# Optimization experiments

Hardware: AMD Instinct MI355X
Metric: run time of the kernel (lower is better)

## Reference

```python
import jax, jax.numpy as jnp
import numpy as np

BETA = 1.0
POWER_ITERS = 9
EPS = 1e-12  # F.normalize default eps


def _normalize(v):
    # L2 normalize over dim=1 of [B, N, 1], matching F.normalize(x, dim=1)
    n = jnp.linalg.norm(v, axis=1, keepdims=True)
    return v / jnp.maximum(n, EPS)


def _dominant_eigenvalue(A, x):
    # A: [B, N, N], x: [B, N, 1]
    for _ in range(POWER_ITERS):
        x = _normalize(jnp.matmul(A, x))
    Ax = jnp.matmul(A, x)[..., 0]              # [B, N]
    num = jnp.sum(Ax * x[..., 0], axis=1)      # x^T A x
    den = jnp.sum(x[..., 0] ** 2, axis=1)      # ||x||^2 (== 1 after normalize)
    return num / den, x


def setup_inputs() -> dict:
    key = jax.random.key(0)
    k1, k2 = jax.random.split(key)
    B, C, H, W = 256, 2048, 7, 7
    x = jax.random.normal(k1, (B, C, H, W), dtype=jnp.float32)
    x0 = _normalize(jax.random.normal(k2, (B, H * W, 1), dtype=jnp.float32))
    return {"x": x, "x0": x0}


def reference(x, x0):
    B, C, H, W = x.shape
    N = H * W
    Wm = x.reshape(B, C, N)
    # ATA = W^T W : [B, N, N]
    ATA = jnp.einsum('bcn,bcm->bnm', Wm, Wm)
    # first power iteration: largest eigenvalue; x0 is a no_grad constant
    largest, x1 = _dominant_eigenvalue(ATA, jax.lax.stop_gradient(x0))
    I = jnp.eye(N, dtype=ATA.dtype)
    shifted = ATA - largest[:, None, None] * I
    # second power iteration warm-started from detached x1 (torch stores last_x detached)
    tmp, _ = _dominant_eigenvalue(shifted, jax.lax.stop_gradient(x1))
    smallest = tmp + largest
    penalty = BETA * (largest / smallest - 1.0) ** 2
    return jnp.sum(penalty) / B
```

## Files before the change

### kernel.cpp

```cpp
#include <hip/hip_runtime.h>
#include <hip/hip_bf16.h>
#include <stdint.h>


#define BATCH 256
#define CDIM  2048
#define NDIM  49
#define QK    512
#define NQ    4
#define CHUNK 64
#define NCHUNK (QK / CHUNK)
#define ITEMS (NDIM * (CHUNK / 8))
#define PSTRIDE 2404

typedef __bf16 bf16x8 __attribute__((ext_vector_type(8)));
typedef float  f32x16 __attribute__((ext_vector_type(16)));
typedef float  f32x4  __attribute__((ext_vector_type(4)));

union V16 {
  f32x4  f4;
  bf16x8 b8;
};

__device__ __forceinline__ void load8(const float* __restrict__ g,
                                      float (&r)[8]) {
#pragma unroll
  for (int j = 0; j < 8; ++j) r[j] = g[j * NDIM];
}

__device__ __forceinline__ void cvt_store(const float (&r)[8], uint32_t* Hb,
                                          uint32_t* Lb, int w) {
  bf16x8 hv, lv;
#pragma unroll
  for (int j = 0; j < 8; ++j) {
    float e = r[j];
    __bf16 h = (__bf16)e;
    hv[j] = h;
    lv[j] = (__bf16)(e - (float)h);
  }
  V16 a, b;
  a.b8 = hv;
  b.b8 = lv;
  *(f32x4*)(Hb + w) = a.f4;
  *(f32x4*)(Lb + w) = b.f4;
}

__device__ __forceinline__ void comp16(const uint32_t* Hb, const uint32_t* Lb,
                                       int m, int n, int hf, f32x16& c1,
                                       f32x16& c2, f32x16& c3) {
  const f32x4* H = (const f32x4*)Hb;
  const f32x4* L = (const f32x4*)Lb;
#pragma unroll
  for (int s = 0; s < 4; ++s) {
    const int blk = 2 * s + hf;
    V16 ah, al, bh, bl;
    ah.f4 = H[m * 8 + (blk ^ (m & 7))];
    al.f4 = L[m * 8 + (blk ^ (m & 7))];
    bh.f4 = H[n * 8 + (blk ^ (n & 7))];
    bl.f4 = L[n * 8 + (blk ^ (n & 7))];
    c1 = __builtin_amdgcn_mfma_f32_32x32x16_bf16(ah.b8, bh.b8, c1, 0, 0, 0);
    c2 = __builtin_amdgcn_mfma_f32_32x32x16_bf16(ah.b8, bl.b8, c2, 0, 0, 0);
    c3 = __builtin_amdgcn_mfma_f32_32x32x16_bf16(al.b8, bh.b8, c3, 0, 0, 0);
  }
}

__global__ __launch_bounds__(256, 4) void gram_kernel(
    const float* __restrict__ x, float* __restrict__ partial,
    float* __restrict__ out) {
  __shared__ __align__(16) uint32_t ldsHi[2][2048];
  __shared__ __align__(16) uint32_t ldsLo[2][2048];

  const int tid  = threadIdx.x;
  const int bidx = blockIdx.x;
  const int batch = bidx >> 2;
  const int q     = bidx & 3;
  const int lane = tid & 63;
  const int wv   = tid >> 6;
  const int ln   = lane & 31;
  const int hf   = lane >> 5;
  const int qm = wv >> 1, qn = wv & 1;
  const int m = qm * 32 + ln;
  const int n = qn * 32 + ln;

  if (bidx == 0 && tid == 0) out[0] = 0.f;

  const float* gbase = x + (size_t)batch * (CDIM * NDIM)
                         + (size_t)q * (QK * NDIM);

  const int i0 = tid;
  const int i1 = tid + 256;
  const bool v1 = (i1 < ITEMS);
  const int kq0 = (i0 * 1338) >> 16;
  const int n0  = i0 - 49 * kq0;
  const int kq1 = (i1 * 1338) >> 16;
  const int n1  = i1 - 49 * kq1;
  const int g0  = kq0 * (8 * NDIM) + n0;
  const int g1  = kq1 * (8 * NDIM) + n1;
  const int w0  = n0 * 32 + 4 * (kq0 ^ (n0 & 7));
  const int w1  = n1 * 32 + 4 * (kq1 ^ (n1 & 7));

  f32x16 c1, c2, c3;
#pragma unroll
  for (int i = 0; i < 16; ++i) { c1[i] = 0.f; c2[i] = 0.f; c3[i] = 0.f; }

  float sA0[8], sA1[8], sB0[8], sB1[8];

  load8(gbase + g0, sA0);
  if (v1) load8(gbase + g1, sA1);

#pragma unroll
  for (int ch = 0; ch < NCHUNK; ch += 2) {
    {
      const float* gch = gbase + (size_t)(ch + 1) * (CHUNK * NDIM);
      load8(gch + g0, sB0);
      if (v1) load8(gch + g1, sB1);
    }
    cvt_store(sA0, ldsHi[0], ldsLo[0], w0);
    if (v1) cvt_store(sA1, ldsHi[0], ldsLo[0], w1);
    __syncthreads();
    comp16(ldsHi[0], ldsLo[0], m, n, hf, c1, c2, c3);

    if (ch + 2 < NCHUNK) {
      const float* gch = gbase + (size_t)(ch + 2) * (CHUNK * NDIM);
      load8(gch + g0, sA0);
      if (v1) load8(gch + g1, sA1);
    }
    cvt_store(sB0, ldsHi[1], ldsLo[1], w0);
    if (v1) cvt_store(sB1, ldsHi[1], ldsLo[1], w1);
    __syncthreads();
    comp16(ldsHi[1], ldsLo[1], m, n, hf, c1, c2, c3);
  }

  float* outp = partial + (size_t)bidx * PSTRIDE;
#pragma unroll
  for (int r = 0; r < 16; ++r) {
    int row = (r & 3) + 8 * (r >> 2) + 4 * hf;
    int mm = qm * 32 + row;
    if (mm < NDIM && n < NDIM)
      outp[mm * NDIM + n] = c1[r] + c2[r] + c3[r];
  }
}

__global__ __launch_bounds__(256) void eigen_kernel(
    const float* __restrict__ partial, const float* __restrict__ x0,
    float* __restrict__ out) {
  __shared__ __align__(16) float A[NDIM * NDIM + 3];

  const int b = blockIdx.x;
  const int t = threadIdx.x;
  const float* p0 = partial + (size_t)(NQ * b) * PSTRIDE;

  const f32x4* q0 = (const f32x4*)(p0);
  const f32x4* q1 = (const f32x4*)(p0 + PSTRIDE);
  const f32x4* q2 = (const f32x4*)(p0 + 2 * PSTRIDE);
  const f32x4* q3 = (const f32x4*)(p0 + 3 * PSTRIDE);
  for (int i = t; i < 600; i += 256) {
    f32x4 s = q0[i] + q1[i] + q2[i] + q3[i];
    ((f32x4*)A)[i] = s;
  }
  if (t == 0)
    A[2400] = p0[2400] + p0[PSTRIDE + 2400] + p0[2 * PSTRIDE + 2400] +
              p0[3 * PSTRIDE + 2400];
  __syncthreads();

  if (t < 64) {
    const bool act = (t < NDIM);
    float Ar[NDIM];
    {
      const float* Arow = &A[(act ? t : (NDIM - 1)) * NDIM];
#pragma unroll
      for (int k = 0; k < NDIM; ++k) Ar[k] = Arow[k];
    }
    float xl = act ? x0[b * NDIM + t] : 0.f;

    auto rayleigh = [&](float shift) -> float {
      for (int it = 0; it < 9; ++it) {
        float a0 = 0.f, a1 = 0.f, a2 = 0.f, a3 = 0.f;
#pragma unroll
        for (int k = 0; k < 48; k += 4) {
          a0 = fmaf(Ar[k + 0], __shfl(xl, k + 0, 64), a0);
          a1 = fmaf(Ar[k + 1], __shfl(xl, k + 1, 64), a1);
          a2 = fmaf(Ar[k + 2], __shfl(xl, k + 2, 64), a2);
          a3 = fmaf(Ar[k + 3], __shfl(xl, k + 3, 64), a3);
        }
        a0 = fmaf(Ar[48], __shfl(xl, 48, 64), a0);
        float y = act ? (((a0 + a1) + (a2 + a3)) - shift * xl) : 0.f;
        float s2 = y * y;
#pragma unroll
        for (int o = 32; o; o >>= 1) s2 += __shfl_xor(s2, o, 64);
        xl = y / fmaxf(sqrtf(s2), 1e-12f);
      }
      float a0 = 0.f, a1 = 0.f, a2 = 0.f, a3 = 0.f;
#pragma unroll
      for (int k = 0; k < 48; k += 4) {
        a0 = fmaf(Ar[k + 0], __shfl(xl, k + 0, 64), a0);
        a1 = fmaf(Ar[k + 1], __shfl(xl, k + 1, 64), a1);
        a2 = fmaf(Ar[k + 2], __shfl(xl, k + 2, 64), a2);
        a3 = fmaf(Ar[k + 3], __shfl(xl, k + 3, 64), a3);
      }
      a0 = fmaf(Ar[48], __shfl(xl, 48, 64), a0);
      float yy = act ? (((a0 + a1) + (a2 + a3)) - shift * xl) : 0.f;
      float num = yy * xl;
      float den = xl * xl;
#pragma unroll
      for (int o = 32; o; o >>= 1) {
        num += __shfl_xor(num, o, 64);
        den += __shfl_xor(den, o, 64);
      }
      return num / den;
    };

    float largest  = rayleigh(0.f);
    float smallest = rayleigh(largest) + largest;
    if (t == 0) {
      float r = largest / smallest - 1.f;
      atomicAdd(out, r * r * (1.0f / (float)BATCH));
    }
  }
}

extern "C" void kernel_launch(void* const* d_in, const int* in_sizes, int n_in,
                              void* d_out, int out_size, void* d_ws,
                              size_t ws_size, hipStream_t stream) {
  const float* x  = (const float*)d_in[0];
  const float* x0 = (const float*)d_in[1];
  float* out = (float*)d_out;
  float* partial = (float*)d_ws;

  gram_kernel<<<1024, 256, 0, stream>>>(x, partial, out);
  eigen_kernel<<<BATCH, 256, 0, stream>>>(partial, x0, out);
}
```

Before: 172.0 us.

## Fuse Gram computation and eigen iteration into one block per batch

Removes the 4-way channel split of the Gram matrix. Each of 256 blocks now computes the full 49x49 Gram matrix for one batch over all 2048 channels, writes it to shared memory, and runs both power iterations in the same kernel. The global partial-sum buffer, the separate eigen kernel and the atomicAdd are gone, replaced by a per-batch penalty array and a small one-block reduction kernel. This saves the partial round trip and a launch, but cuts the grid from 1024 to 256 blocks, which lowers parallelism for the memory-bound Gram phase. Each block also runs a serial loop four times longer.

New measurement: 172.8 us. No clear change (+0.5%).

```diff
diff --git a/kernel.cpp b/kernel.cpp
--- a/kernel.cpp
+++ b/kernel.cpp
@@ -6,12 +6,10 @@
 #define BATCH 256
 #define CDIM  2048
 #define NDIM  49
-#define QK    512
-#define NQ    4
 #define CHUNK 64
-#define NCHUNK (QK / CHUNK)
+#define NCHUNK (CDIM / CHUNK)
 #define ITEMS (NDIM * (CHUNK / 8))
-#define PSTRIDE 2404
+#define CHUNK_FLOATS (CHUNK * NDIM)
 
 typedef __bf16 bf16x8 __attribute__((ext_vector_type(8)));
 typedef float  f32x16 __attribute__((ext_vector_type(16)));
@@ -64,16 +62,15 @@
   }
 }
 
-__global__ __launch_bounds__(256, 4) void gram_kernel(
-    const float* __restrict__ x, float* __restrict__ partial,
-    float* __restrict__ out) {
+__global__ __launch_bounds__(256) void fused_kernel(
+    const float* __restrict__ x, const float* __restrict__ x0,
+    float* __restrict__ pen) {
   __shared__ __align__(16) uint32_t ldsHi[2][2048];
   __shared__ __align__(16) uint32_t ldsLo[2][2048];
+  __shared__ __align__(16) float A[NDIM * NDIM + 3];
 
   const int tid  = threadIdx.x;
-  const int bidx = blockIdx.x;
-  const int batch = bidx >> 2;
-  const int q     = bidx & 3;
+  const int b    = blockIdx.x;
   const int lane = tid & 63;
   const int wv   = tid >> 6;
   const int ln   = lane & 31;
@@ -82,10 +79,7 @@
   const int m = qm * 32 + ln;
   const int n = qn * 32 + ln;
 
-  if (bidx == 0 && tid == 0) out[0] = 0.f;
-
-  const float* gbase = x + (size_t)batch * (CDIM * NDIM)
-                         + (size_t)q * (QK * NDIM);
+  const float* gbase = x + (size_t)b * (CDIM * NDIM);
 
   const int i0 = tid;
   const int i1 = tid + 256;
@@ -108,10 +102,9 @@
   load8(gbase + g0, sA0);
   if (v1) load8(gbase + g1, sA1);
 
-#pragma unroll
   for (int ch = 0; ch < NCHUNK; ch += 2) {
     {
-      const float* gch = gbase + (size_t)(ch + 1) * (CHUNK * NDIM);
+      const float* gch = gbase + (size_t)(ch + 1) * CHUNK_FLOATS;
       load8(gch + g0, sB0);
       if (v1) load8(gch + g1, sB1);
     }
@@ -121,7 +114,7 @@
     comp16(ldsHi[0], ldsLo[0], m, n, hf, c1, c2, c3);
 
     if (ch + 2 < NCHUNK) {
-      const float* gch = gbase + (size_t)(ch + 2) * (CHUNK * NDIM);
+      const float* gch = gbase + (size_t)(ch + 2) * CHUNK_FLOATS;
       load8(gch + g0, sA0);
       if (v1) load8(gch + g1, sA1);
     }
@@ -131,47 +124,24 @@
     comp16(ldsHi[1], ldsLo[1], m, n, hf, c1, c2, c3);
   }
 
-  float* outp = partial + (size_t)bidx * PSTRIDE;
 #pragma unroll
   for (int r = 0; r < 16; ++r) {
     int row = (r & 3) + 8 * (r >> 2) + 4 * hf;
     int mm = qm * 32 + row;
     if (mm < NDIM && n < NDIM)
-      outp[mm * NDIM + n] = c1[r] + c2[r] + c3[r];
-  }
-}
-
-__global__ __launch_bounds__(256) void eigen_kernel(
-    const float* __restrict__ partial, const float* __restrict__ x0,
-    float* __restrict__ out) {
-  __shared__ __align__(16) float A[NDIM * NDIM + 3];
-
-  const int b = blockIdx.x;
-  const int t = threadIdx.x;
-  const float* p0 = partial + (size_t)(NQ * b) * PSTRIDE;
-
-  const f32x4* q0 = (const f32x4*)(p0);
-  const f32x4* q1 = (const f32x4*)(p0 + PSTRIDE);
-  const f32x4* q2 = (const f32x4*)(p0 + 2 * PSTRIDE);
-  const f32x4* q3 = (const f32x4*)(p0 + 3 * PSTRIDE);
-  for (int i = t; i < 600; i += 256) {
-    f32x4 s = q0[i] + q1[i] + q2[i] + q3[i];
-    ((f32x4*)A)[i] = s;
-  }
-  if (t == 0)
-    A[2400] = p0[2400] + p0[PSTRIDE + 2400] + p0[2 * PSTRIDE + 2400] +
-              p0[3 * PSTRIDE + 2400];
+      A[mm * NDIM + n] = c1[r] + c2[r] + c3[r];
+  }
   __syncthreads();
 
-  if (t < 64) {
-    const bool act = (t < NDIM);
+  if (tid < 64) {
+    const bool act = (tid < NDIM);
     float Ar[NDIM];
     {
-      const float* Arow = &A[(act ? t : (NDIM - 1)) * NDIM];
+      const float* Arow = &A[(act ? tid : (NDIM - 1)) * NDIM];
 #pragma unroll
       for (int k = 0; k < NDIM; ++k) Ar[k] = Arow[k];
     }
-    float xl = act ? x0[b * NDIM + t] : 0.f;
+    float xl = act ? x0[b * NDIM + tid] : 0.f;
 
     auto rayleigh = [&](float shift) -> float {
       for (int it = 0; it < 9; ++it) {
@@ -212,11 +182,20 @@
 
     float largest  = rayleigh(0.f);
     float smallest = rayleigh(largest) + largest;
-    if (t == 0) {
+    if (tid == 0) {
       float r = largest / smallest - 1.f;
-      atomicAdd(out, r * r * (1.0f / (float)BATCH));
-    }
-  }
+      pen[b] = r * r;
+    }
+  }
+}
+
+__global__ __launch_bounds__(64) void finish_kernel(
+    const float* __restrict__ pen, float* __restrict__ out) {
+  const int t = threadIdx.x;
+  float s = pen[t] + pen[t + 64] + pen[t + 128] + pen[t + 192];
+#pragma unroll
+  for (int o = 32; o; o >>= 1) s += __shfl_xor(s, o, 64);
+  if (t == 0) out[0] = s * (1.0f / (float)BATCH);
 }
 
 extern "C" void kernel_launch(void* const* d_in, const int* in_sizes, int n_in,
@@ -225,8 +204,8 @@
   const float* x  = (const float*)d_in[0];
   const float* x0 = (const float*)d_in[1];
   float* out = (float*)d_out;
-  float* partial = (float*)d_ws;
-
-  gram_kernel<<<1024, 256, 0, stream>>>(x, partial, out);
-  eigen_kernel<<<BATCH, 256, 0, stream>>>(partial, x0, out);
-}
+  float* pen = (float*)d_ws;
+
+  fused_kernel<<<BATCH, 256, 0, stream>>>(x, x0, pen);
+  finish_kernel<<<1, 64, 0, stream>>>(pen, out);
+}
```
